# Kernel tuning notes

Measured on AMD Instinct MI355X. Metric: run time of the kernel, lower is better.

## Reference

```python
import jax, jax.numpy as jnp
import numpy as np

DT = 0.1
DN = ('NCHW', 'OIHW', 'NCHW')

LAP = jnp.array([[1., 2., 1.], [2., -12., 2.], [1., 2., 1.]], jnp.float32)
SOBEL_X = jnp.array([[-1., 0., 1.], [-2., 0., 2.], [-1., 0., 1.]], jnp.float32)
LAP_K = (LAP / 12.0)[None, None]  # [1,1,3,3], zero-padded laplacian kernel


def conv_lap(x):
    # 3x3 laplacian/12 conv with zero padding=1 on a single-channel map
    return jax.lax.conv_general_dilated(x, LAP_K, (1, 1), ((1, 1), (1, 1)), dimension_numbers=DN)


def conv1x1(x, w, b=None):
    # w: [O, C]
    y = jnp.einsum('bchw,oc->bohw', x, w)
    if b is not None:
        y = y + b[None, :, None, None]
    return y


def avg_pool5(x):
    # torch avg_pool2d(5,1,2) with count_include_pad=True -> always divide by 25
    s = jax.lax.reduce_window(x, 0.0, jax.lax.add, (1, 1, 5, 5), (1, 1, 1, 1),
                              [(0, 0), (0, 0), (2, 2), (2, 2)])
    return s / 25.0


def min_pool3(x):
    # -maxpool(-x) in torch == min-pool with +inf padding
    return jax.lax.reduce_window(x, jnp.inf, jax.lax.min, (1, 1, 3, 3), (1, 1, 1, 1),
                                 [(0, 0), (0, 0), (1, 1), (1, 1)])


def perception(x):
    # reduced_perception(x, 0): depthwise circular 3x3 conv with [sobel_x, sobel_x.T, lap]
    B, C, H, W = x.shape
    filters = jnp.stack([SOBEL_X, SOBEL_X.T, LAP])        # [3,3,3]
    k = jnp.tile(filters, (C, 1, 1))[:, None]              # [3C,1,3,3]; per-channel groups of 3
    xp = jnp.pad(x, ((0, 0), (0, 0), (1, 1), (1, 1)), mode='wrap')
    obs = jax.lax.conv_general_dilated(xp, k, (1, 1), 'VALID',
                                       feature_group_count=C, dimension_numbers=DN)
    return jnp.concatenate([x, obs], axis=1)               # [B, 4C, H, W]


def setup_inputs() -> dict:
    key = jax.random.key(0)
    ks = jax.random.split(key, 10)
    B, C, H, W = 16, 21, 256, 256
    hidden_n, gene_size = 96, 3
    return {
        'x': jax.random.uniform(ks[0], (B, C, H, W), jnp.float32),
        'rand_noise': jax.random.uniform(ks[1], (B, 1, H, W), jnp.float32),
        'w1_w': jax.random.normal(ks[2], (hidden_n, 4 * C), jnp.float32) * 0.05,
        'w1_b': jax.random.normal(ks[3], (hidden_n,), jnp.float32) * 0.02,
        'w2_w': jax.random.normal(ks[4], (gene_size, hidden_n), jnp.float32) * 0.05,
        'slow_w': jax.random.normal(ks[5], (3, 5), jnp.float32) * 0.1,
        'slow_b': jax.random.normal(ks[6], (3,), jnp.float32) * 0.02,
        'mod_w': jax.random.normal(ks[7], (3, 3), jnp.float32) * 0.1,
        'mod_b': jax.random.normal(ks[8], (3,), jnp.float32) * 0.02,
        'alpha': jnp.float32(0.1),
        'beta': jnp.float32(0.1),
        'omega': jnp.float32(0.0),
        'K': jnp.float32(0.5),
        'kappa': jnp.float32(0.5),
    }


def reference(x, rand_noise, w1_w, w1_b, w2_w, slow_w, slow_b, mod_w, mod_b,
              alpha, beta, omega, K, kappa):
    # step=0, k=4 -> slow (reaction-diffusion) branch executes; update_rate=0.5
    prefix = x[:, :12]
    gene = x[:, 12:15]
    a = x[:, 15:16]
    b = x[:, 16:17]
    d = x[:, 17:18]

    # slow_perception on rgba + hidden
    alpha_ch = x[:, 3:4]
    eroded = min_pool3(alpha_ch)
    Q = jnp.concatenate([alpha_ch, alpha_ch - eroded, conv_lap(alpha_ch), x[:, 4:6]], axis=1)  # 5 ch
    I = conv1x1(Q, slow_w, slow_b)
    Ia, Ib, Id = I[:, 0:1], I[:, 1:2], I[:, 2:3]

    # discrete reaction-diffusion update
    new_a = a + DT * (-alpha * a + omega * b + K * conv_lap(a) + Ia)
    new_b = b + DT * (-alpha * b - omega * a + K * conv_lap(b) + Ib)
    new_d = d + DT * (-beta * d + kappa * conv_lap(d) + Id)

    # local consensus update
    a_avg = avg_pool5(new_a)
    b_avg = avg_pool5(new_b)
    rho = jnp.sqrt(a_avg ** 2 + b_avg ** 2 + 1e-6)
    a_avg = a_avg / rho
    b_avg = b_avg / rho
    new_a = new_a + DT * (a_avg - new_a)
    new_b = new_b + DT * (b_avg - new_b)

    # ring attractor phases (variable naming follows the source's swapped unpack)
    phase = jnp.sqrt(new_a ** 2 + new_b ** 2 + 1e-6)  # local amplitude
    amplitude = jnp.arctan2(new_b, new_a)             # local angle
    a, b, d = new_a, new_b, new_d

    mod = conv1x1(jnp.concatenate([a, b, d], axis=1), mod_w, mod_b)

    # gene update MLP over full perception
    y = conv1x1(jax.nn.relu(conv1x1(perception(x), w1_w, w1_b)), w2_w)

    update_mask = jnp.floor(rand_noise + 0.5)
    xmp = jnp.pad(x[:, 3:4], ((0, 0), (0, 0), (1, 1), (1, 1)), mode='wrap')
    life = (jax.lax.reduce_window(xmp, -jnp.inf, jax.lax.max, (1, 1, 3, 3), (1, 1, 1, 1),
                                  'VALID') > 0.1).astype(x.dtype)
    new_gene = gene + y * update_mask * life

    x_final = jnp.concatenate([prefix, new_gene, a, b, d, mod], axis=1)
    return x_final, phase, amplitude
```

## Files before the change

### kernel.cpp

```cpp
#include <hip/hip_runtime.h>
#include <math.h>

#define HH 256
#define WW 256
#define CC 21
#define BB 16
#define HW (HH*WW)
#define CHW (CC*HW)
#define PHASE_OFF (BB*CHW)
#define AMP_OFF (PHASE_OFF + BB*HW)

static constexpr float DT = 0.1f;

typedef short short8 __attribute__((ext_vector_type(8)));
typedef float floatx4 __attribute__((ext_vector_type(4)));

__device__ __forceinline__ unsigned f2bf_bits(float f) {
    unsigned u = __builtin_bit_cast(unsigned, f);
    return (u + 0x7fffu + ((u >> 16) & 1u)) >> 16;
}
__device__ __forceinline__ float bf2f(short s) {
    unsigned u = ((unsigned)(unsigned short)s) << 16;
    return __builtin_bit_cast(float, u);
}

__global__ __launch_bounds__(256)
void k0_prep(const float* __restrict__ w1w, short* __restrict__ w1p) {
    const int i = blockIdx.x * 256 + threadIdx.x;
    if (i >= 96 * 96) return;
    const int h = i / 96, kk = i - h * 96;
    const int c = kk >> 2, f = kk & 3;
    float v = 0.f;
    if (c < 21) {
        const int orig = (f == 0) ? c : (21 + 3 * c + (f - 1));
        v = w1w[h * 84 + orig];
    }
    w1p[i] = (short)f2bf_bits(v);
}

__global__ __launch_bounds__(256)
void k12_react(const float* __restrict__ x,
               const float* __restrict__ slow_w, const float* __restrict__ slow_b,
               const float* __restrict__ mod_w, const float* __restrict__ mod_b,
               const float* __restrict__ alpha_p, const float* __restrict__ beta_p,
               const float* __restrict__ omega_p, const float* __restrict__ K_p,
               const float* __restrict__ kappa_p,
               float* __restrict__ out)
{
    __shared__ float t[6][14][38];
    __shared__ float na[12][36], nb[12][36];

    const int tx = threadIdx.x, ty = threadIdx.y;
    const int bb = blockIdx.z;
    const int X0 = blockIdx.x * 32, Y0 = blockIdx.y * 8;
    const int tid = ty * 32 + tx;

    const float alpha = alpha_p[0], beta = beta_p[0], omega = omega_p[0];
    const float Kc = K_p[0], kappa = kappa_p[0];

    const int chs[6] = {3, 4, 5, 15, 16, 17};
    for (int i = tid; i < 6 * 532; i += 256) {
        const int ch = i / 532;
        const int rem = i - ch * 532;
        const int r = rem / 38, c = rem - r * 38;
        const int gy = Y0 + r - 3, gx = X0 + c - 3;
        const bool inb = (gy >= 0) && (gy < HH) && (gx >= 0) && (gx < WW);
        t[ch][r][c] = inb ? x[((bb * CC + chs[ch]) * HH + gy) * WW + gx] : 0.f;
    }
    __syncthreads();

    for (int i = tid; i < 432; i += 256) {
        const int r2 = i / 36, c2 = i - r2 * 36;
        const int gy = Y0 + r2 - 2, gx = X0 + c2 - 2;
        float va = 0.f, vb = 0.f;
        if (gy >= 0 && gy < HH && gx >= 0 && gx < WW) {
            const int lr = r2 + 1, lc = c2 + 1;
            float lap3 = 0.f, lapA = 0.f, lapB = 0.f, emin = INFINITY;
            #pragma unroll
            for (int dy = -1; dy <= 1; dy++) {
                #pragma unroll
                for (int dx = -1; dx <= 1; dx++) {
                    const float lw = ((dy == 0 && dx == 0) ? -12.f
                                     : ((dy == 0 || dx == 0) ? 2.f : 1.f)) * (1.f / 12.f);
                    const float v3 = t[0][lr + dy][lc + dx];
                    lap3 = fmaf(lw, v3, lap3);
                    lapA = fmaf(lw, t[3][lr + dy][lc + dx], lapA);
                    lapB = fmaf(lw, t[4][lr + dy][lc + dx], lapB);
                    const bool nin = (gy + dy >= 0) && (gy + dy < HH) && (gx + dx >= 0) && (gx + dx < WW);
                    emin = fminf(emin, nin ? v3 : INFINITY);
                }
            }
            const float Q0 = t[0][lr][lc];
            const float Q1 = Q0 - emin, Q2 = lap3;
            const float Q3 = t[1][lr][lc], Q4 = t[2][lr][lc];
            const float I0 = slow_b[0] + slow_w[0] * Q0 + slow_w[1] * Q1 + slow_w[2] * Q2 + slow_w[3] * Q3 + slow_w[4] * Q4;
            const float I1 = slow_b[1] + slow_w[5] * Q0 + slow_w[6] * Q1 + slow_w[7] * Q2 + slow_w[8] * Q3 + slow_w[9] * Q4;
            const float a = t[3][lr][lc], b = t[4][lr][lc];
            va = a + DT * (-alpha * a + omega * b + Kc * lapA + I0);
            vb = b + DT * (-alpha * b - omega * a + Kc * lapB + I1);
        }
        na[r2][c2] = va;
        nb[r2][c2] = vb;
    }
    __syncthreads();

    const int gy = Y0 + ty, gx = X0 + tx;
    const int lr = ty + 3, lc = tx + 3;

    float sa = 0.f, sb = 0.f;
    #pragma unroll
    for (int dy = 0; dy < 5; dy++)
        #pragma unroll
        for (int dx = 0; dx < 5; dx++) {
            sa += na[ty + dy][tx + dx];
            sb += nb[ty + dy][tx + dx];
        }
    sa *= (1.f / 25.f); sb *= (1.f / 25.f);
    const float rho = sqrtf(sa * sa + sb * sb + 1e-6f);
    const float an = sa / rho, bn = sb / rho;
    const float a0 = na[ty + 2][tx + 2], b0 = nb[ty + 2][tx + 2];
    const float A2 = a0 + DT * (an - a0);
    const float B2 = b0 + DT * (bn - b0);

    float lapD = 0.f, lap3 = 0.f, emin = INFINITY;
    #pragma unroll
    for (int dy = -1; dy <= 1; dy++)
        #pragma unroll
        for (int dx = -1; dx <= 1; dx++) {
            const float lw = ((dy == 0 && dx == 0) ? -12.f
                             : ((dy == 0 || dx == 0) ? 2.f : 1.f)) * (1.f / 12.f);
            lapD = fmaf(lw, t[5][lr + dy][lc + dx], lapD);
            const float v3 = t[0][lr + dy][lc + dx];
            lap3 = fmaf(lw, v3, lap3);
            const bool nin = (gy + dy >= 0) && (gy + dy < HH) && (gx + dx >= 0) && (gx + dx < WW);
            emin = fminf(emin, nin ? v3 : INFINITY);
        }
    const float Q0 = t[0][lr][lc];
    const float I2 = slow_b[2] + slow_w[10] * Q0 + slow_w[11] * (Q0 - emin) + slow_w[12] * lap3
                   + slow_w[13] * t[1][lr][lc] + slow_w[14] * t[2][lr][lc];
    const float d0 = t[5][lr][lc];
    const float nd = d0 + DT * (-beta * d0 + kappa * lapD + I2);

    const float ph = sqrtf(A2 * A2 + B2 * B2 + 1e-6f);
    const float am = atan2f(B2, A2);

    const int po = gy * WW + gx;
    float* ob = out + bb * CHW;
    ob[15 * HW + po] = A2;
    ob[16 * HW + po] = B2;
    ob[17 * HW + po] = nd;
    #pragma unroll
    for (int j = 0; j < 3; j++)
        ob[(18 + j) * HW + po] = mod_b[j] + mod_w[j * 3 + 0] * A2 + mod_w[j * 3 + 1] * B2 + mod_w[j * 3 + 2] * nd;
    out[PHASE_OFF + bb * HW + po] = ph;
    out[AMP_OFF + bb * HW + po] = am;
}

__global__ __launch_bounds__(256, 2)
void k3_gene(const float* __restrict__ x, const float* __restrict__ noise,
             const short* __restrict__ w1p, const float* __restrict__ w1b,
             const float* __restrict__ w2w,
             float* __restrict__ out)
{
    __shared__ __align__(16) short P[256 * 96];
    __shared__ float xt[CC][10][34];

    const int tx = threadIdx.x & 31;
    const int ty = (threadIdx.y * blockDim.x + threadIdx.x) >> 5;
    const int tid = threadIdx.y * 32 + threadIdx.x;
    const int bb = blockIdx.z;
    const int X0 = blockIdx.x * 32, Y0 = blockIdx.y * 8;
    const float* xb = x + bb * CHW;

    for (int i = tid; i < CC * 340; i += 256) {
        const int c = i / 340;
        const int rem = i - c * 340;
        const int r = rem / 34;
        const int cc = rem - r * 34;
        const int yy = (Y0 + r - 1) & (HH - 1);
        const int xx = (X0 + cc - 1) & (WW - 1);
        (&xt[0][0][0])[i] = xb[c * HW + yy * WW + xx];
    }
    __syncthreads();

    const int lx = tx + 1, ly = ty + 1;
    #pragma unroll
    for (int c = 0; c < CC; c++) {
        const float n00 = xt[c][ly - 1][lx - 1], n01 = xt[c][ly - 1][lx], n02 = xt[c][ly - 1][lx + 1];
        const float n10 = xt[c][ly][lx - 1],     n11 = xt[c][ly][lx],     n12 = xt[c][ly][lx + 1];
        const float n20 = xt[c][ly + 1][lx - 1], n21 = xt[c][ly + 1][lx], n22 = xt[c][ly + 1][lx + 1];
        const float fid = n11;
        const float fsx = (n02 - n00) + 2.f * (n12 - n10) + (n22 - n20);
        const float fsy = (n20 - n00) + 2.f * (n21 - n01) + (n22 - n02);
        const float flap = (n00 + n02 + n20 + n22) + 2.f * (n01 + n10 + n12 + n21) - 12.f * n11;
        const unsigned lo = f2bf_bits(fid) | (f2bf_bits(fsx) << 16);
        const unsigned hi = f2bf_bits(fsy) | (f2bf_bits(flap) << 16);
        unsigned* dst = (unsigned*)(P + tid * 96 + 4 * c);
        *(uint2*)dst = make_uint2(lo, hi);
    }
    {
        unsigned* dst = (unsigned*)(P + tid * 96 + 84);
        *(uint2*)(dst)     = make_uint2(0u, 0u);
        *(uint2*)(dst + 2) = make_uint2(0u, 0u);
        *(uint2*)(dst + 4) = make_uint2(0u, 0u);
    }

    float m = xt[3][ly - 1][lx - 1];
    m = fmaxf(m, xt[3][ly - 1][lx]); m = fmaxf(m, xt[3][ly - 1][lx + 1]);
    m = fmaxf(m, xt[3][ly][lx - 1]); m = fmaxf(m, xt[3][ly][lx]); m = fmaxf(m, xt[3][ly][lx + 1]);
    m = fmaxf(m, xt[3][ly + 1][lx - 1]); m = fmaxf(m, xt[3][ly + 1][lx]); m = fmaxf(m, xt[3][ly + 1][lx + 1]);
    const float life = (m > 0.1f) ? 1.f : 0.f;
    const int gy = Y0 + ty, gx = X0 + tx;
    const int po = gy * WW + gx;
    const float g = floorf(noise[bb * HW + po] + 0.5f) * life;
    const float c12 = xt[12][ly][lx], c13 = xt[13][ly][lx], c14 = xt[14][ly][lx];

    float* ob = out + bb * CHW;
    #pragma unroll
    for (int c = 0; c < 12; c++) ob[c * HW + po] = xt[c][ly][lx];
    __syncthreads();

    {
        const int w = tid >> 6;
        const int lane = tid & 63;
        const int ln = lane & 15;
        const int kg = lane >> 4;

        float bias[6];
        #pragma unroll
        for (int nt = 0; nt < 6; nt++) bias[nt] = w1b[nt * 16 + ln];

        short8 bfr[18];
        #pragma unroll
        for (int nt = 0; nt < 6; nt++)
            #pragma unroll
            for (int ks = 0; ks < 3; ks++)
                bfr[nt * 3 + ks] = *(const short8*)(w1p + (nt * 16 + ln) * 96 + ks * 32 + kg * 8);

        #pragma unroll
        for (int mt = 0; mt < 4; mt++) {
            const int m0 = w * 64 + mt * 16;
            const short* arow = P + (m0 + ln) * 96 + kg * 8;
            const short8 a0 = *(const short8*)(arow);
            const short8 a1 = *(const short8*)(arow + 32);
            const short8 a2 = *(const short8*)(arow + 64);

            floatx4 acc[6];
            #pragma unroll
            for (int nt = 0; nt < 6; nt++) {
                floatx4 c4 = {0.f, 0.f, 0.f, 0.f};
                c4 = __builtin_amdgcn_mfma_f32_16x16x32_bf16(a0, bfr[nt * 3 + 0], c4, 0, 0, 0);
                c4 = __builtin_amdgcn_mfma_f32_16x16x32_bf16(a1, bfr[nt * 3 + 1], c4, 0, 0, 0);
                c4 = __builtin_amdgcn_mfma_f32_16x16x32_bf16(a2, bfr[nt * 3 + 2], c4, 0, 0, 0);
                acc[nt] = c4;
            }
            #pragma unroll
            for (int nt = 0; nt < 6; nt++)
                #pragma unroll
                for (int r = 0; r < 4; r++) {
                    float h = acc[nt][r] + bias[nt];
                    h = fmaxf(h, 0.f);
                    P[(m0 + kg * 4 + r) * 96 + nt * 16 + ln] = (short)f2bf_bits(h);
                }
        }
    }
    __syncthreads();

    float y0 = 0.f, y1 = 0.f, y2 = 0.f;
    const short* hrow = P + tid * 96;
    #pragma unroll
    for (int gq = 0; gq < 12; gq++) {
        const short8 hv = *(const short8*)(hrow + gq * 8);
        #pragma unroll
        for (int j = 0; j < 8; j++) {
            const float h = bf2f(hv[j]);
            y0 = fmaf(w2w[gq * 8 + j], h, y0);
            y1 = fmaf(w2w[96 + gq * 8 + j], h, y1);
            y2 = fmaf(w2w[192 + gq * 8 + j], h, y2);
        }
    }
    ob[12 * HW + po] = c12 + y0 * g;
    ob[13 * HW + po] = c13 + y1 * g;
    ob[14 * HW + po] = c14 + y2 * g;
}

extern "C" void kernel_launch(void* const* d_in, const int* in_sizes, int n_in,
                              void* d_out, int out_size, void* d_ws, size_t ws_size,
                              hipStream_t stream)
{
    const float* x      = (const float*)d_in[0];
    const float* noise  = (const float*)d_in[1];
    const float* w1w    = (const float*)d_in[2];
    const float* w1b    = (const float*)d_in[3];
    const float* w2w    = (const float*)d_in[4];
    const float* sloww  = (const float*)d_in[5];
    const float* slowb  = (const float*)d_in[6];
    const float* modw   = (const float*)d_in[7];
    const float* modb   = (const float*)d_in[8];
    const float* alphap = (const float*)d_in[9];
    const float* betap  = (const float*)d_in[10];
    const float* omegap = (const float*)d_in[11];
    const float* Kp     = (const float*)d_in[12];
    const float* kappap = (const float*)d_in[13];
    float* out = (float*)d_out;

    short* w1p = (short*)d_ws;

    dim3 blk(32, 8, 1);
    dim3 grd(WW / 32, HH / 8, BB);

    k0_prep<<<dim3(36), dim3(256), 0, stream>>>(w1w, w1p);
    k12_react<<<grd, blk, 0, stream>>>(x, sloww, slowb, modw, modb,
                                       alphap, betap, omegap, Kp, kappap, out);
    k3_gene<<<grd, blk, 0, stream>>>(x, noise, w1p, w1b, w2w, out);
}
```

Before: 314.7 us.

## Fold perception stencils into first-layer weights and fuse second layer into MFMA epilogue

Instead of computing the sobel/laplacian perception features per pixel and then running the MLP, the first-layer weights are pre-combined with the 3x3 stencils into nine shifted weight slices. The gene kernel then runs MFMAs directly on a bf16 channels-last halo tile, and the relu and second layer are reduced in registers with wave shuffles. This removes the large LDS staging buffer for perception and hidden activations, shrinking shared memory and raising occupancy to 4 blocks per CU, in exchange for three times more MFMA work. The react kernel's 5x5 average pool is also made separable through a horizontal-sum shared buffer. Identity channels and life max now read bf16-rounded inputs, which slightly changes precision.

Result: slower. 394.0 us (+25.2%).

```diff
diff --git a/kernel.cpp b/kernel.cpp
--- a/kernel.cpp
+++ b/kernel.cpp
@@ -25,17 +25,30 @@
 }
 
 __global__ __launch_bounds__(256)
-void k0_prep(const float* __restrict__ w1w, short* __restrict__ w1p) {
+void k0_prep(const float* __restrict__ w1w, const float* __restrict__ w1b,
+             const float* __restrict__ w2w,
+             short* __restrict__ weff, float4* __restrict__ w2b)
+{
+    const float SX[9] = {-1.f, 0.f, 1.f, -2.f, 0.f, 2.f, -1.f, 0.f, 1.f};
+    const float SY[9] = {-1.f, -2.f, -1.f, 0.f, 0.f, 0.f, 1.f, 2.f, 1.f};
+    const float LP[9] = {1.f, 2.f, 1.f, 2.f, -12.f, 2.f, 1.f, 2.f, 1.f};
     const int i = blockIdx.x * 256 + threadIdx.x;
-    if (i >= 96 * 96) return;
-    const int h = i / 96, kk = i - h * 96;
-    const int c = kk >> 2, f = kk & 3;
-    float v = 0.f;
-    if (c < 21) {
-        const int orig = (f == 0) ? c : (21 + 3 * c + (f - 1));
-        v = w1w[h * 84 + orig];
-    }
-    w1p[i] = (short)f2bf_bits(v);
+    if (i < 9 * 96 * 32) {
+        const int s = i / (96 * 32);
+        const int rem = i - s * 96 * 32;
+        const int n = rem >> 5, c = rem & 31;
+        float v = 0.f;
+        if (c < 21) {
+            v = w1w[n * 84 + c] * ((s == 4) ? 1.f : 0.f)
+              + w1w[n * 84 + 21 + 3 * c + 0] * SX[s]
+              + w1w[n * 84 + 21 + 3 * c + 1] * SY[s]
+              + w1w[n * 84 + 21 + 3 * c + 2] * LP[s];
+        }
+        weff[i] = (short)f2bf_bits(v);
+    } else if (i < 9 * 96 * 32 + 96) {
+        const int n = i - 9 * 96 * 32;
+        w2b[n] = make_float4(w2w[n], w2w[96 + n], w2w[192 + n], w1b[n]);
+    }
 }
 
 __global__ __launch_bounds__(256)
@@ -49,6 +62,7 @@
 {
     __shared__ float t[6][14][38];
     __shared__ float na[12][36], nb[12][36];
+    __shared__ float ha[12][32], hb[12][32];
 
     const int tx = threadIdx.x, ty = threadIdx.y;
     const int bb = blockIdx.z;
@@ -104,17 +118,21 @@
     }
     __syncthreads();
 
+    for (int i = tid; i < 384; i += 256) {
+        const int r = i >> 5, c = i & 31;
+        float sa = 0.f, sb = 0.f;
+        #pragma unroll
+        for (int dx = 0; dx < 5; dx++) { sa += na[r][c + dx]; sb += nb[r][c + dx]; }
+        ha[r][c] = sa; hb[r][c] = sb;
+    }
+    __syncthreads();
+
     const int gy = Y0 + ty, gx = X0 + tx;
     const int lr = ty + 3, lc = tx + 3;
 
     float sa = 0.f, sb = 0.f;
     #pragma unroll
-    for (int dy = 0; dy < 5; dy++)
-        #pragma unroll
-        for (int dx = 0; dx < 5; dx++) {
-            sa += na[ty + dy][tx + dx];
-            sb += nb[ty + dy][tx + dx];
-        }
+    for (int dy = 0; dy < 5; dy++) { sa += ha[ty + dy][tx]; sb += hb[ty + dy][tx]; }
     sa *= (1.f / 25.f); sb *= (1.f / 25.f);
     const float rho = sqrtf(sa * sa + sb * sb + 1e-6f);
     const float an = sa / rho, bn = sb / rho;
@@ -156,132 +174,126 @@
     out[AMP_OFF + bb * HW + po] = am;
 }
 
-__global__ __launch_bounds__(256, 2)
+__global__ __launch_bounds__(256, 4)
 void k3_gene(const float* __restrict__ x, const float* __restrict__ noise,
-             const short* __restrict__ w1p, const float* __restrict__ w1b,
-             const float* __restrict__ w2w,
+             const short* __restrict__ weff, const float4* __restrict__ w2b,
              float* __restrict__ out)
 {
-    __shared__ __align__(16) short P[256 * 96];
-    __shared__ float xt[CC][10][34];
-
-    const int tx = threadIdx.x & 31;
-    const int ty = (threadIdx.y * blockDim.x + threadIdx.x) >> 5;
-    const int tid = threadIdx.y * 32 + threadIdx.x;
+    __shared__ __align__(16) short xt[10][34][40];
+
+    const int tx = threadIdx.x, ty = threadIdx.y;
+    const int tid = ty * 32 + tx;
+    const int w = tid >> 6, lane = tid & 63;
+    const int ln = lane & 15, kg = lane >> 4;
     const int bb = blockIdx.z;
     const int X0 = blockIdx.x * 32, Y0 = blockIdx.y * 8;
     const float* xb = x + bb * CHW;
 
-    for (int i = tid; i < CC * 340; i += 256) {
-        const int c = i / 340;
-        const int rem = i - c * 340;
-        const int r = rem / 34;
-        const int cc = rem - r * 34;
-        const int yy = (Y0 + r - 1) & (HH - 1);
-        const int xx = (X0 + cc - 1) & (WW - 1);
-        (&xt[0][0][0])[i] = xb[c * HW + yy * WW + xx];
+    for (int idx = tid; idx < 340; idx += 256) {
+        const int r = idx / 34, cc = idx - r * 34;
+        const int gy = (Y0 + r - 1) & (HH - 1);
+        const int gxx = (X0 + cc - 1) & (WW - 1);
+        const float* src = xb + gy * WW + gxx;
+        short* dst = &xt[r][cc][0];
+        #pragma unroll
+        for (int c = 0; c < 20; c += 2) {
+            const unsigned lo = f2bf_bits(src[c * HW]);
+            const unsigned hi = f2bf_bits(src[(c + 1) * HW]);
+            *(unsigned*)(dst + c) = lo | (hi << 16);
+        }
+        *(unsigned*)(dst + 20) = f2bf_bits(src[20 * HW]);
+        #pragma unroll
+        for (int c = 22; c < 40; c += 2) *(unsigned*)(dst + c) = 0u;
     }
     __syncthreads();
 
-    const int lx = tx + 1, ly = ty + 1;
-    #pragma unroll
-    for (int c = 0; c < CC; c++) {
-        const float n00 = xt[c][ly - 1][lx - 1], n01 = xt[c][ly - 1][lx], n02 = xt[c][ly - 1][lx + 1];
-        const float n10 = xt[c][ly][lx - 1],     n11 = xt[c][ly][lx],     n12 = xt[c][ly][lx + 1];
-        const float n20 = xt[c][ly + 1][lx - 1], n21 = xt[c][ly + 1][lx], n22 = xt[c][ly + 1][lx + 1];
-        const float fid = n11;
-        const float fsx = (n02 - n00) + 2.f * (n12 - n10) + (n22 - n20);
-        const float fsy = (n20 - n00) + 2.f * (n21 - n01) + (n22 - n02);
-        const float flap = (n00 + n02 + n20 + n22) + 2.f * (n01 + n10 + n12 + n21) - 12.f * n11;
-        const unsigned lo = f2bf_bits(fid) | (f2bf_bits(fsx) << 16);
-        const unsigned hi = f2bf_bits(fsy) | (f2bf_bits(flap) << 16);
-        unsigned* dst = (unsigned*)(P + tid * 96 + 4 * c);
-        *(uint2*)dst = make_uint2(lo, hi);
-    }
-    {
-        unsigned* dst = (unsigned*)(P + tid * 96 + 84);
-        *(uint2*)(dst)     = make_uint2(0u, 0u);
-        *(uint2*)(dst + 2) = make_uint2(0u, 0u);
-        *(uint2*)(dst + 4) = make_uint2(0u, 0u);
-    }
-
-    float m = xt[3][ly - 1][lx - 1];
-    m = fmaxf(m, xt[3][ly - 1][lx]); m = fmaxf(m, xt[3][ly - 1][lx + 1]);
-    m = fmaxf(m, xt[3][ly][lx - 1]); m = fmaxf(m, xt[3][ly][lx]); m = fmaxf(m, xt[3][ly][lx + 1]);
-    m = fmaxf(m, xt[3][ly + 1][lx - 1]); m = fmaxf(m, xt[3][ly + 1][lx]); m = fmaxf(m, xt[3][ly + 1][lx + 1]);
-    const float life = (m > 0.1f) ? 1.f : 0.f;
     const int gy = Y0 + ty, gx = X0 + tx;
     const int po = gy * WW + gx;
+    float* ob = out + bb * CHW;
+    const float* xc = xb + po;
+    #pragma unroll
+    for (int c = 0; c < 12; c++) ob[c * HW + po] = xc[c * HW];
+    const float c12 = xc[12 * HW], c13 = xc[13 * HW], c14 = xc[14 * HW];
+
+    float m = -1e30f;
+    #pragma unroll
+    for (int ky = 0; ky < 3; ky++)
+        #pragma unroll
+        for (int kx = 0; kx < 3; kx++)
+            m = fmaxf(m, bf2f(xt[ty + ky][tx + kx][3]));
+    const float life = (m > 0.1f) ? 1.f : 0.f;
     const float g = floorf(noise[bb * HW + po] + 0.5f) * life;
-    const float c12 = xt[12][ly][lx], c13 = xt[13][ly][lx], c14 = xt[14][ly][lx];
-
-    float* ob = out + bb * CHW;
-    #pragma unroll
-    for (int c = 0; c < 12; c++) ob[c * HW + po] = xt[c][ly][lx];
-    __syncthreads();
-
-    {
-        const int w = tid >> 6;
-        const int lane = tid & 63;
-        const int ln = lane & 15;
-        const int kg = lane >> 4;
-
-        float bias[6];
-        #pragma unroll
-        for (int nt = 0; nt < 6; nt++) bias[nt] = w1b[nt * 16 + ln];
-
-        short8 bfr[18];
-        #pragma unroll
-        for (int nt = 0; nt < 6; nt++)
-            #pragma unroll
-            for (int ks = 0; ks < 3; ks++)
-                bfr[nt * 3 + ks] = *(const short8*)(w1p + (nt * 16 + ln) * 96 + ks * 32 + kg * 8);
-
-        #pragma unroll
-        for (int mt = 0; mt < 4; mt++) {
-            const int m0 = w * 64 + mt * 16;
-            const short* arow = P + (m0 + ln) * 96 + kg * 8;
-            const short8 a0 = *(const short8*)(arow);
-            const short8 a1 = *(const short8*)(arow + 32);
-            const short8 a2 = *(const short8*)(arow + 64);
-
-            floatx4 acc[6];
-            #pragma unroll
-            for (int nt = 0; nt < 6; nt++) {
-                floatx4 c4 = {0.f, 0.f, 0.f, 0.f};
-                c4 = __builtin_amdgcn_mfma_f32_16x16x32_bf16(a0, bfr[nt * 3 + 0], c4, 0, 0, 0);
-                c4 = __builtin_amdgcn_mfma_f32_16x16x32_bf16(a1, bfr[nt * 3 + 1], c4, 0, 0, 0);
-                c4 = __builtin_amdgcn_mfma_f32_16x16x32_bf16(a2, bfr[nt * 3 + 2], c4, 0, 0, 0);
-                acc[nt] = c4;
-            }
-            #pragma unroll
-            for (int nt = 0; nt < 6; nt++)
+
+    const short* xtf = &xt[0][0][0];
+    int aoff[4];
+    #pragma unroll
+    for (int mt = 0; mt < 4; mt++)
+        aoff[mt] = ((2 * w + (mt >> 1)) * 34 + (mt & 1) * 16 + ln) * 40 + kg * 8;
+
+    float yj0[4] = {0.f, 0.f, 0.f, 0.f};
+    float yj1[4] = {0.f, 0.f, 0.f, 0.f};
+    float yj2[4] = {0.f, 0.f, 0.f, 0.f};
+
+    #pragma unroll
+    for (int pass = 0; pass < 2; pass++) {
+        floatx4 acc[4][3];
+        #pragma unroll
+        for (int mt = 0; mt < 4; mt++)
+            #pragma unroll
+            for (int nt = 0; nt < 3; nt++)
+                acc[mt][nt] = (floatx4){0.f, 0.f, 0.f, 0.f};
+
+        #pragma unroll
+        for (int s = 0; s < 9; s++) {
+            const int soff = ((s / 3) * 34 + (s % 3)) * 40;
+            short8 af[4];
+            #pragma unroll
+            for (int mt = 0; mt < 4; mt++)
+                af[mt] = *(const short8*)(xtf + aoff[mt] + soff);
+            short8 bf[3];
+            #pragma unroll
+            for (int nt = 0; nt < 3; nt++)
+                bf[nt] = *(const short8*)(weff + ((size_t)(s * 96 + pass * 48 + nt * 16 + ln)) * 32 + kg * 8);
+            #pragma unroll
+            for (int nt = 0; nt < 3; nt++)
+                #pragma unroll
+                for (int mt = 0; mt < 4; mt++)
+                    acc[mt][nt] = __builtin_amdgcn_mfma_f32_16x16x32_bf16(bf[nt], af[mt], acc[mt][nt], 0, 0, 0);
+        }
+
+        #pragma unroll
+        for (int nt = 0; nt < 3; nt++) {
+            float4 wb[4];
+            #pragma unroll
+            for (int r = 0; r < 4; r++)
+                wb[r] = w2b[pass * 48 + nt * 16 + kg * 4 + r];
+            #pragma unroll
+            for (int mt = 0; mt < 4; mt++)
                 #pragma unroll
                 for (int r = 0; r < 4; r++) {
-                    float h = acc[nt][r] + bias[nt];
-                    h = fmaxf(h, 0.f);
-                    P[(m0 + kg * 4 + r) * 96 + nt * 16 + ln] = (short)f2bf_bits(h);
+                    const float h = fmaxf(acc[mt][nt][r] + wb[r].w, 0.f);
+                    yj0[mt] = fmaf(h, wb[r].x, yj0[mt]);
+                    yj1[mt] = fmaf(h, wb[r].y, yj1[mt]);
+                    yj2[mt] = fmaf(h, wb[r].z, yj2[mt]);
                 }
         }
     }
-    __syncthreads();
-
-    float y0 = 0.f, y1 = 0.f, y2 = 0.f;
-    const short* hrow = P + tid * 96;
-    #pragma unroll
-    for (int gq = 0; gq < 12; gq++) {
-        const short8 hv = *(const short8*)(hrow + gq * 8);
-        #pragma unroll
-        for (int j = 0; j < 8; j++) {
-            const float h = bf2f(hv[j]);
-            y0 = fmaf(w2w[gq * 8 + j], h, y0);
-            y1 = fmaf(w2w[96 + gq * 8 + j], h, y1);
-            y2 = fmaf(w2w[192 + gq * 8 + j], h, y2);
-        }
-    }
-    ob[12 * HW + po] = c12 + y0 * g;
-    ob[13 * HW + po] = c13 + y1 * g;
-    ob[14 * HW + po] = c14 + y2 * g;
+
+    float fy0 = 0.f, fy1 = 0.f, fy2 = 0.f;
+    #pragma unroll
+    for (int mt = 0; mt < 4; mt++) {
+        float t0 = yj0[mt] + __shfl_xor(yj0[mt], 16, 64);
+        t0 += __shfl_xor(t0, 32, 64);
+        float t1 = yj1[mt] + __shfl_xor(yj1[mt], 16, 64);
+        t1 += __shfl_xor(t1, 32, 64);
+        float t2 = yj2[mt] + __shfl_xor(yj2[mt], 16, 64);
+        t2 += __shfl_xor(t2, 32, 64);
+        if (kg == mt) { fy0 = t0; fy1 = t1; fy2 = t2; }
+    }
+
+    ob[12 * HW + po] = c12 + fy0 * g;
+    ob[13 * HW + po] = c13 + fy1 * g;
+    ob[14 * HW + po] = c14 + fy2 * g;
 }
 
 extern "C" void kernel_launch(void* const* d_in, const int* in_sizes, int n_in,
@@ -304,13 +316,14 @@
     const float* kappap = (const float*)d_in[13];
     float* out = (float*)d_out;
 
-    short* w1p = (short*)d_ws;
+    short* weff = (short*)d_ws;
+    float4* w2b = (float4*)((char*)d_ws + 55296);
 
     dim3 blk(32, 8, 1);
     dim3 grd(WW / 32, HH / 8, BB);
 
-    k0_prep<<<dim3(36), dim3(256), 0, stream>>>(w1w, w1p);
+    k0_prep<<<dim3(109), dim3(256), 0, stream>>>(w1w, w1b, w2w, weff, w2b);
     k12_react<<<grd, blk, 0, stream>>>(x, sloww, slowb, modw, modb,
                                        alphap, betap, omegap, Kp, kappap, out);
-    k3_gene<<<grd, blk, 0, stream>>>(x, noise, w1p, w1b, w2w, out);
-}
+    k3_gene<<<grd, blk, 0, stream>>>(x, noise, weff, w2b, out);
+}
```
